# Kernel optimization log

Measured on AMD Instinct MI355X. Metric: run time of the kernel, lower is better.

Reference implementation:

```python
import jax, jax.numpy as jnp
import numpy as np

OUT, IN = 11008, 4096  # LLaMA-7B FFN up-projection


def _unpack(packed, shape):
    """Unpack 2-bit fields (4 ternary values per byte, stored as q+1 in {0,1,2})."""
    shifts = jnp.arange(4, dtype=packed.dtype) * 2
    vals = (packed[:, None] >> shifts) & 3            # [n_bytes, 4]
    n = shape[0] * shape[1]
    q = vals.reshape(-1)[:n].astype(jnp.float32) - 1.0  # back to {-1,0,1}
    return q.reshape(shape)


def _pack(q):
    """Pack ternary int values {-1,0,1} -> 2-bit fields, 4 per byte."""
    flat = (q + 1).reshape(-1)
    pad = (-flat.shape[0]) % 4
    flat = jnp.pad(flat, (0, pad))
    groups = flat.reshape(-1, 4)
    weights = (jnp.int32(1) << (jnp.arange(4, dtype=jnp.int32) * 2))
    return jnp.sum(groups * weights, axis=1).astype(jnp.int32)


def setup_inputs() -> dict:
    key = jax.random.key(0)
    kx, kw = jax.random.split(key)
    x = jax.random.normal(kx, (4, 2048, IN), dtype=jnp.float32)
    # build a realistic weight, then absmean-quantize it (per output row)
    W = jax.random.normal(kw, (OUT, IN), dtype=jnp.float32) * 0.02
    weight_scale = jnp.mean(jnp.abs(W), axis=1, keepdims=True)  # [OUT, 1]
    q = jnp.clip(jnp.round(W / weight_scale), -1.0, 1.0).astype(jnp.int32)
    packed_weight = _pack(q)  # [OUT*IN/4] int32 bytes
    return {"x": x, "packed_weight": packed_weight, "weight_scale": weight_scale}


def reference(x, packed_weight, weight_scale):
    # unpack ternary weights, dequantize via per-row scale, dense GEMM
    W = _unpack(packed_weight, (OUT, IN)) * weight_scale  # [OUT, IN] fp32
    return jnp.einsum('bsi,oi->bso', x, W)
```

## Files before the change

### kernel.cpp

```cpp
#include <hip/hip_runtime.h>
#include <hip/hip_bf16.h>


#define M_DIM 8192
#define N_DIM 11008
#define K_DIM 4096
#define BM 128
#define BN 256
#define BK 64
#define KT 64
#define NB_N (N_DIM / BN)
#define NWG ((M_DIM / BM) * NB_N)

#define XBF_BYTES ((size_t)M_DIM * K_DIM * 2)
#define BT_BYTES  ((size_t)N_DIM * K_DIM / 4)
#define WS_NEED   (XBF_BYTES + BT_BYTES)

typedef __attribute__((ext_vector_type(8))) short bf16x8;
typedef __attribute__((ext_vector_type(4))) float f32x4;

__device__ inline unsigned int bf16b(float f) {
  union { __hip_bfloat16 h; unsigned short u; } cv;
  cv.h = __float2bfloat16(f);
  return (unsigned int)cv.u;
}

__device__ __forceinline__ void gload_lds16(const void* g, void* l) {
  __builtin_amdgcn_global_load_lds(
      (const __attribute__((address_space(1))) unsigned int*)g,
      (__attribute__((address_space(3))) unsigned int*)l, 16, 0, 0);
}

#define XCVT_BLOCKS 16384
#define PACK_BLOCKS 5504
__global__ __launch_bounds__(256)
void prep_kernel(const float* __restrict__ X, const int* __restrict__ PW,
                 unsigned short* __restrict__ Xbf, unsigned char* __restrict__ Bt) {
  const int b = blockIdx.x;
  if (b < XCVT_BLOCKS) {
    const size_t i8 = ((size_t)b * 256 + threadIdx.x) * 8;
    float4 a = *(const float4*)(X + i8);
    float4 c = *(const float4*)(X + i8 + 4);
    uint4 o;
    o.x = bf16b(a.x) | (bf16b(a.y) << 16);
    o.y = bf16b(a.z) | (bf16b(a.w) << 16);
    o.z = bf16b(c.x) | (bf16b(c.y) << 16);
    o.w = bf16b(c.z) | (bf16b(c.w) << 16);
    *(uint4*)(Xbf + i8) = o;
  } else {
    const size_t i8 = ((size_t)(b - XCVT_BLOCKS) * 256 + threadIdx.x) * 8;
    int4 p = *(const int4*)(PW + i8);
    int4 q = *(const int4*)(PW + i8 + 4);
    uint2 o;
    o.x = (unsigned)(p.x & 255) | ((unsigned)(p.y & 255) << 8) |
          ((unsigned)(p.z & 255) << 16) | ((unsigned)(p.w & 255) << 24);
    o.y = (unsigned)(q.x & 255) | ((unsigned)(q.y & 255) << 8) |
          ((unsigned)(q.z & 255) << 16) | ((unsigned)(q.w & 255) << 24);
    *(uint2*)(Bt + i8) = o;
  }
}

__global__ __launch_bounds__(256, 2)
void qlin_main_kernel(const unsigned short* __restrict__ Xbf,
                      const unsigned char* __restrict__ Bt,
                      const float* __restrict__ SC, float* __restrict__ OUT) {
  __shared__ unsigned short As[2][BM * BK];
  __shared__ unsigned char  Bs[2][BN * 16];

  const int tid = threadIdx.x;
  const int lane = tid & 63;
  const int w = tid >> 6;

  const int wg = blockIdx.x;
  const int swz = (wg & 7) * (NWG / 8) + (wg >> 3);
  const int bm = swz / NB_N;
  const int bn = swz - bm * NB_N;

  const int l3 = lane >> 3;
  const int asrc_c = (lane & 7) ^ l3;
  const char* ab0 = (const char*)Xbf +
      (size_t)(bm * BM + w * 32 + l3) * (K_DIM * 2) + asrc_c * 16;
  const char* bb = (const char*)Bt + (size_t)(bn * BN + w * 64 + lane) * (K_DIM / 4);

  unsigned short* adst0 = &As[0][w * 2048];
  unsigned short* adst1 = &As[1][w * 2048];
  unsigned char* bdst0 = &Bs[0][w * 1024];
  unsigned char* bdst1 = &Bs[1][w * 1024];

#define STAGE(AD, BD, KT_) do {                                   \
    gload_lds16(ab0 + (KT_)*128,              (AD));              \
    gload_lds16(ab0 + (KT_)*128 + 1*65536,    (AD) + 512);        \
    gload_lds16(ab0 + (KT_)*128 + 2*65536,    (AD) + 1024);       \
    gload_lds16(ab0 + (KT_)*128 + 3*65536,    (AD) + 1536);       \
    gload_lds16(bb  + (KT_)*16,               (BD));              \
  } while (0)

  f32x4 acc[8][4];
#pragma unroll
  for (int i = 0; i < 8; ++i)
#pragma unroll
    for (int j = 0; j < 4; ++j) acc[i][j] = (f32x4){0.f, 0.f, 0.f, 0.f};

  const int l4 = lane >> 4;
  const int axor = lane & 7;
  const int arow = (lane & 15) * 128;
  const int hb = l4 >> 1;
  const unsigned hoff = (unsigned)(l4 & 1) * 16;
  const int rbase = (w * 64 + (lane & 15)) * 16 + hb * 4;

#define COMPUTE(B_) do {                                                        \
    _Pragma("unroll")                                                           \
    for (int kk = 0; kk < 2; ++kk) {                                            \
      bf16x8 af[8];                                                             \
      _Pragma("unroll")                                                         \
      for (int m = 0; m < 8; ++m)                                               \
        af[m] = *(const bf16x8*)((const char*)As[B_] + m * 2048 + arow +        \
                                 (((kk * 4 + l4) ^ axor) << 4));                \
      _Pragma("unroll")                                                         \
      for (int n = 0; n < 4; ++n) {                                             \
        const unsigned d = *(const unsigned*)(&Bs[B_][rbase + n * 256 + kk * 8]); \
        const unsigned w16 = (d >> hoff) & 0xFFFFu;                             \
        const unsigned u = w16 | (w16 << 14);                                   \
        union { uint4 s; bf16x8 v; } bfr;                                       \
        bfr.s.x = ((u << 14) & 0xC000C000u) + 0x40004000u;                      \
        bfr.s.y = ((u << 10) & 0xC000C000u) + 0x40004000u;                      \
        bfr.s.z = ((u << 6)  & 0xC000C000u) + 0x40004000u;                      \
        bfr.s.w = ((u << 2)  & 0xC000C000u) + 0x40004000u;                      \
        _Pragma("unroll")                                                       \
        for (int m = 0; m < 8; ++m)                                             \
          acc[m][n] = __builtin_amdgcn_mfma_f32_16x16x32_bf16(af[m], bfr.v,     \
                                                              acc[m][n], 0, 0, 0); \
      }                                                                         \
    }                                                                           \
  } while (0)

  STAGE(adst0, bdst0, 0);
  __syncthreads();
  for (int kt = 0; kt < KT; kt += 2) {
    STAGE(adst1, bdst1, kt + 1);
    COMPUTE(0);
    __syncthreads();
    if (kt + 2 < KT) STAGE(adst0, bdst0, kt + 2);
    COMPUTE(1);
    __syncthreads();
  }
#undef STAGE
#undef COMPUTE

  const int gc0 = bn * BN + w * 64 + (lane & 15);
  const int gr0 = bm * BM + (l4 << 2);
  float sc[4];
#pragma unroll
  for (int n = 0; n < 4; ++n) sc[n] = -0.5f * SC[gc0 + n * 16];
#pragma unroll
  for (int m = 0; m < 8; ++m)
#pragma unroll
    for (int n = 0; n < 4; ++n)
#pragma unroll
      for (int r = 0; r < 4; ++r)
        OUT[(size_t)(gr0 + m * 16 + r) * N_DIM + gc0 + n * 16] = acc[m][n][r] * sc[n];
}

#define BSTRIDE 20
__global__ __launch_bounds__(256, 2)
void qlin_fused_kernel(const float* __restrict__ X, const int* __restrict__ PW,
                       const float* __restrict__ SC, float* __restrict__ OUT) {
  __shared__ unsigned short Asf[BM * BK];
  __shared__ unsigned char Bp[BN * BSTRIDE];

  const int tid = threadIdx.x;
  const int wg = blockIdx.x;
  const int swz = (wg & 7) * (NWG / 8) + (wg >> 3);
  const int bm = swz / NB_N;
  const int bn = swz - bm * NB_N;

  const int lane = tid & 63;
  const int wave = tid >> 6;
  const int wr = wave >> 1;
  const int wc = wave & 1;

  const int arow = tid >> 3;
  const int ac8  = tid & 7;
  const float* xptr = X + (size_t)(bm * BM + arow) * K_DIM + ac8 * 8;
  const unsigned int aswz = ((unsigned)arow & 7u) << 4;

  const int bc  = tid & 3;
  const int br0 = tid >> 2;
  const int* pwptr = PW + (size_t)(bn * BN + br0) * (K_DIM / 4) + bc * 4;
  const int bwoff = (bc & 1) * 8 + (bc >> 1) * 2;

  f32x4 acc[4][8];
#pragma unroll
  for (int i = 0; i < 4; ++i)
#pragma unroll
    for (int j = 0; j < 8; ++j) acc[i][j] = (f32x4){0.f, 0.f, 0.f, 0.f};

  float4 av[4][2];
  int4 bv[4];
#pragma unroll
  for (int j = 0; j < 4; ++j) {
    av[j][0] = *(const float4*)(xptr + (size_t)(32 * j) * K_DIM);
    av[j][1] = *(const float4*)(xptr + (size_t)(32 * j) * K_DIM + 4);
  }
#pragma unroll
  for (int j = 0; j < 4; ++j)
    bv[j] = *(const int4*)(pwptr + (size_t)(64 * j) * (K_DIM / 4));

  for (int kt = 0; kt < KT; ++kt) {
    __syncthreads();
#pragma unroll
    for (int j = 0; j < 4; ++j) {
      uint4 wv;
      wv.x = bf16b(av[j][0].x) | (bf16b(av[j][0].y) << 16);
      wv.y = bf16b(av[j][0].z) | (bf16b(av[j][0].w) << 16);
      wv.z = bf16b(av[j][1].x) | (bf16b(av[j][1].y) << 16);
      wv.w = bf16b(av[j][1].z) | (bf16b(av[j][1].w) << 16);
      *(uint4*)((char*)Asf + (arow + 32 * j) * 128 + (((unsigned)ac8 * 16u) ^ aswz)) = wv;
    }
#pragma unroll
    for (int j = 0; j < 4; ++j) {
      const unsigned int ulo = ((unsigned)bv[j].x & 255u) | (((unsigned)bv[j].y & 255u) << 8);
      const unsigned int uhi = ((unsigned)bv[j].z & 255u) | (((unsigned)bv[j].w & 255u) << 8);
      unsigned char* dst = Bp + (br0 + 64 * j) * BSTRIDE + bwoff;
      *(unsigned short*)(dst)     = (unsigned short)ulo;
      *(unsigned short*)(dst + 4) = (unsigned short)uhi;
    }
    __syncthreads();

    if (kt + 1 < KT) {
#pragma unroll
      for (int j = 0; j < 4; ++j) {
        av[j][0] = *(const float4*)(xptr + (kt + 1) * BK + (size_t)(32 * j) * K_DIM);
        av[j][1] = *(const float4*)(xptr + (kt + 1) * BK + (size_t)(32 * j) * K_DIM + 4);
      }
#pragma unroll
      for (int j = 0; j < 4; ++j)
        bv[j] = *(const int4*)(pwptr + (kt + 1) * 16 + (size_t)(64 * j) * (K_DIM / 4));
    }

    const int bh = lane >> 4;
    const int bcol0 = wc * 128 + (lane & 15);
    unsigned int d[8];
#pragma unroll
    for (int n = 0; n < 8; ++n)
      d[n] = *(const unsigned int*)(Bp + (bcol0 + n * 16) * BSTRIDE + bh * 4);

    const unsigned int rswz = ((unsigned)lane & 7u) << 4;
#pragma unroll
    for (int kk = 0; kk < 2; ++kk) {
      bf16x8 af[4];
      const unsigned int coff = (((unsigned)(kk * 4 + (lane >> 4))) * 16u) ^ rswz;
#pragma unroll
      for (int m = 0; m < 4; ++m)
        af[m] = *(const bf16x8*)((const char*)Asf + (wr * 64 + m * 16 + (lane & 15)) * 128 + coff);
#pragma unroll
      for (int n = 0; n < 8; ++n) {
        const unsigned int w16 = kk ? (d[n] >> 16) : (d[n] & 0xFFFFu);
        const unsigned int u = w16 | (w16 << 14);
        union { uint4 s; bf16x8 v; } bfr;
        bfr.s.x = ((u << 14) & 0xC000C000u) + 0x40004000u;
        bfr.s.y = ((u << 10) & 0xC000C000u) + 0x40004000u;
        bfr.s.z = ((u << 6)  & 0xC000C000u) + 0x40004000u;
        bfr.s.w = ((u << 2)  & 0xC000C000u) + 0x40004000u;
#pragma unroll
        for (int m = 0; m < 4; ++m)
          acc[m][n] = __builtin_amdgcn_mfma_f32_16x16x32_bf16(af[m], bfr.v, acc[m][n], 0, 0, 0);
      }
    }
  }

  const int gc0 = bn * BN + wc * 128 + (lane & 15);
  const int gr0 = bm * BM + wr * 64 + ((lane >> 4) << 2);
  float sc[8];
#pragma unroll
  for (int n = 0; n < 8; ++n) sc[n] = -0.5f * SC[gc0 + n * 16];
#pragma unroll
  for (int m = 0; m < 4; ++m)
#pragma unroll
    for (int n = 0; n < 8; ++n)
#pragma unroll
      for (int r = 0; r < 4; ++r)
        OUT[(size_t)(gr0 + m * 16 + r) * N_DIM + gc0 + n * 16] = acc[m][n][r] * sc[n];
}

extern "C" void kernel_launch(void* const* d_in, const int* in_sizes, int n_in,
                              void* d_out, int out_size, void* d_ws, size_t ws_size,
                              hipStream_t stream) {
  const float* x  = (const float*)d_in[0];
  const int*   pw = (const int*)d_in[1];
  const float* sc = (const float*)d_in[2];
  float* out = (float*)d_out;
  (void)in_sizes; (void)n_in; (void)out_size;

  if (ws_size >= WS_NEED) {
    unsigned short* xbf = (unsigned short*)d_ws;
    unsigned char* bt = (unsigned char*)d_ws + XBF_BYTES;
    prep_kernel<<<dim3(XCVT_BLOCKS + PACK_BLOCKS), dim3(256), 0, stream>>>(x, pw, xbf, bt);
    qlin_main_kernel<<<dim3(NWG), dim3(256), 0, stream>>>(xbf, bt, sc, out);
  } else {
    qlin_fused_kernel<<<dim3(NWG), dim3(256), 0, stream>>>(x, pw, sc, out);
  }
}
```

Before: 704.3 us.

## Switch to triple-buffered LDS pipeline with one barrier per k-tile

```diff
diff --git a/kernel.cpp b/kernel.cpp
--- a/kernel.cpp
+++ b/kernel.cpp
@@ -64,8 +64,8 @@
 void qlin_main_kernel(const unsigned short* __restrict__ Xbf,
                       const unsigned char* __restrict__ Bt,
                       const float* __restrict__ SC, float* __restrict__ OUT) {
-  __shared__ unsigned short As[2][BM * BK];
-  __shared__ unsigned char  Bs[2][BN * 16];
+  __shared__ unsigned short As[3][BM * BK];
+  __shared__ unsigned char  Bs[3][BN * 16];
 
   const int tid = threadIdx.x;
   const int lane = tid & 63;
@@ -82,17 +82,14 @@
       (size_t)(bm * BM + w * 32 + l3) * (K_DIM * 2) + asrc_c * 16;
   const char* bb = (const char*)Bt + (size_t)(bn * BN + w * 64 + lane) * (K_DIM / 4);
 
-  unsigned short* adst0 = &As[0][w * 2048];
-  unsigned short* adst1 = &As[1][w * 2048];
-  unsigned char* bdst0 = &Bs[0][w * 1024];
-  unsigned char* bdst1 = &Bs[1][w * 1024];
-
-#define STAGE(AD, BD, KT_) do {                                   \
-    gload_lds16(ab0 + (KT_)*128,              (AD));              \
-    gload_lds16(ab0 + (KT_)*128 + 1*65536,    (AD) + 512);        \
-    gload_lds16(ab0 + (KT_)*128 + 2*65536,    (AD) + 1024);       \
-    gload_lds16(ab0 + (KT_)*128 + 3*65536,    (AD) + 1536);       \
-    gload_lds16(bb  + (KT_)*16,               (BD));              \
+#define STAGE(IDX, KT_) do {                                           \
+    unsigned short* ad_ = &As[IDX][w * 2048];                          \
+    unsigned char* bd_ = &Bs[IDX][w * 1024];                           \
+    gload_lds16(ab0 + (KT_)*128,           ad_);                       \
+    gload_lds16(ab0 + (KT_)*128 + 65536,   ad_ + 512);                 \
+    gload_lds16(ab0 + (KT_)*128 + 131072,  ad_ + 1024);                \
+    gload_lds16(ab0 + (KT_)*128 + 196608,  ad_ + 1536);                \
+    gload_lds16(bb  + (KT_)*16,            bd_);                       \
   } while (0)
 
   f32x4 acc[8][4];
@@ -109,16 +106,18 @@
   const int rbase = (w * 64 + (lane & 15)) * 16 + hb * 4;
 
 #define COMPUTE(B_) do {                                                        \
+    const char* asb_ = (const char*)&As[B_][0];                                 \
+    const unsigned char* bsb_ = &Bs[B_][0];                                     \
     _Pragma("unroll")                                                           \
     for (int kk = 0; kk < 2; ++kk) {                                            \
       bf16x8 af[8];                                                             \
       _Pragma("unroll")                                                         \
       for (int m = 0; m < 8; ++m)                                               \
-        af[m] = *(const bf16x8*)((const char*)As[B_] + m * 2048 + arow +        \
+        af[m] = *(const bf16x8*)(asb_ + m * 2048 + arow +                       \
                                  (((kk * 4 + l4) ^ axor) << 4));                \
       _Pragma("unroll")                                                         \
       for (int n = 0; n < 4; ++n) {                                             \
-        const unsigned d = *(const unsigned*)(&Bs[B_][rbase + n * 256 + kk * 8]); \
+        const unsigned d = *(const unsigned*)(bsb_ + rbase + n * 256 + kk * 8); \
         const unsigned w16 = (d >> hoff) & 0xFFFFu;                             \
         const unsigned u = w16 | (w16 << 14);                                   \
         union { uint4 s; bf16x8 v; } bfr;                                       \
@@ -134,16 +133,21 @@
     }                                                                           \
   } while (0)
 
-  STAGE(adst0, bdst0, 0);
-  __syncthreads();
-  for (int kt = 0; kt < KT; kt += 2) {
-    STAGE(adst1, bdst1, kt + 1);
-    COMPUTE(0);
-    __syncthreads();
-    if (kt + 2 < KT) STAGE(adst0, bdst0, kt + 2);
-    COMPUTE(1);
-    __syncthreads();
-  }
+  STAGE(0, 0);
+  int cur = 0;
+  for (int kt = 0; kt < KT - 1; ++kt) {
+    const int nxt = (cur == 2) ? 0 : cur + 1;
+    STAGE(nxt, kt + 1);
+    asm volatile("s_waitcnt vmcnt(5)" ::: "memory");
+    asm volatile("s_waitcnt lgkmcnt(0)" ::: "memory");
+    __builtin_amdgcn_s_barrier();
+    COMPUTE(cur);
+    cur = nxt;
+  }
+  asm volatile("s_waitcnt vmcnt(0)" ::: "memory");
+  asm volatile("s_waitcnt lgkmcnt(0)" ::: "memory");
+  __builtin_amdgcn_s_barrier();
+  COMPUTE(cur);
 #undef STAGE
 #undef COMPUTE
 
```

New measurement: 637.6 us. -9.5%, faster.
